# Kernel optimization log

Measured on AMD Instinct MI355X. Metric: run time of the kernel, lower is better.

## Reference

```python
import jax, jax.numpy as jnp
import numpy as np

VOCAB = 1276   # medical-code vocab (one_hot depth for word)
AGE_DEPTH = 91 # one_hot depth for age


def setup_inputs() -> dict:
    key = jax.random.key(0)
    k1, k2, k3 = jax.random.split(key, 3)
    B, S, BAG, D = 64, 128, 40, 768
    word = jax.random.randint(k1, (B, S, BAG), 0, VOCAB)
    age = jax.random.randint(k2, (B, S), 0, AGE_DEPTH)
    W = jax.random.normal(k3, (VOCAB + AGE_DEPTH, D), dtype=jnp.float32) * 0.02
    b = jnp.zeros((D,), dtype=jnp.float32)
    return {"word": word, "age": age, "W": W, "b": b}


def reference(word, age, W, b):
    # word: [B, S, BAG] int codes; age: [B, S] int.
    B, S, BAG = word.shape
    # Multi-hot count-sum: equivalent to reduce_sum(one_hot(word, VOCAB), axis=-2)
    # but computed via scatter-add, avoiding the dense [B,S,BAG,VOCAB] tensor.
    flat = word.reshape(B * S, BAG)
    offs = jnp.arange(B * S, dtype=word.dtype)[:, None] * VOCAB
    counts = (
        jnp.zeros((B * S * VOCAB,), jnp.float32)
        .at[(flat + offs).ravel()]
        .add(1.0)
        .reshape(B, S, VOCAB)
    )
    year = jax.nn.one_hot(age, AGE_DEPTH, dtype=jnp.float32)  # [B, S, 91]
    x = jnp.concatenate([counts, year], axis=-1)              # [B, S, 1367]
    return x @ W + b                                          # [B, S, 768]
```

## Files before the change

kernel.cpp:

```cpp
#include <hip/hip_runtime.h>
#include <hip/hip_fp16.h>

constexpr int BAG       = 40;
constexpr int D         = 768;
constexpr int VOCAB     = 1276;
constexpr int AGE_DEPTH = 91;
constexpr int WROWS     = VOCAB + AGE_DEPTH;

constexpr int COLS = 16;
constexpr int NSLC = D / COLS;
constexpr int RPB  = 256;
constexpr int TPB  = 512;
constexpr int LDSU = 2 * WROWS;

typedef float fx4 __attribute__((ext_vector_type(4)));

__device__ __forceinline__ __half2 u2h(uint u) {
    union { uint u; __half2 h; } v; v.u = u; return v.h;
}
__device__ __forceinline__ ushort f2h(float f) {
    __half h = __float2half(f);
    return *reinterpret_cast<ushort*>(&h);
}

__global__ __launch_bounds__(256) void convert_w_f16(
    const float* __restrict__ W, ushort* __restrict__ Wh, int n)
{
    const int i = (blockIdx.x * 256 + threadIdx.x) * 8;
    if (i + 8 > n) return;
    const float4 a = *reinterpret_cast<const float4*>(W + i);
    const float4 b = *reinterpret_cast<const float4*>(W + i + 4);
    uint4 p;
    p.x = (uint)f2h(a.x) | ((uint)f2h(a.y) << 16);
    p.y = (uint)f2h(a.z) | ((uint)f2h(a.w) << 16);
    p.z = (uint)f2h(b.x) | ((uint)f2h(b.y) << 16);
    p.w = (uint)f2h(b.z) | ((uint)f2h(b.w) << 16);
    *reinterpret_cast<uint4*>(Wh + i) = p;
}

__global__ __launch_bounds__(TPB) void embed_lds_kernel(
    const int* __restrict__ word,
    const int* __restrict__ age,
    const ushort* __restrict__ Wh,
    const float* __restrict__ bias,
    float* __restrict__ out)
{
    __shared__ uint4 lds4[LDSU];

    const int rb = blockIdx.x;
    const int c0 = blockIdx.y * COLS;

    const int t     = threadIdx.x;
    const int chunk = t & 1;
    const int rloc  = t >> 1;
    const int row   = rb * RPB + rloc;

    const int* __restrict__ wrow = word + row * BAG;

    for (int s = t; s < LDSU; s += TPB) {
        const int r = s >> 1;
        const int u = s & 1;
        lds4[u * WROWS + r] =
            *reinterpret_cast<const uint4*>(Wh + (size_t)r * D + c0 + u * 8);
    }

    const int aidx = VOCAB + age[row];
    int cur[8];
    {
        const int4 q0 = *reinterpret_cast<const int4*>(wrow);
        const int4 q1 = *reinterpret_cast<const int4*>(wrow + 4);
        cur[0]=q0.x; cur[1]=q0.y; cur[2]=q0.z; cur[3]=q0.w;
        cur[4]=q1.x; cur[5]=q1.y; cur[6]=q1.z; cur[7]=q1.w;
    }

    __syncthreads();

    const uint4* __restrict__ lp = lds4 + chunk * WROWS;

    __half2 a0 = u2h(0u), a1 = u2h(0u), a2 = u2h(0u), a3 = u2h(0u);

    #pragma unroll
    for (int kb = 0; kb < 5; ++kb) {
        uint4 g[8];
        #pragma unroll
        for (int u = 0; u < 8; ++u)
            g[u] = lp[cur[u]];

        int nxt[8];
        if (kb < 4) {
            const int4 q0 = *reinterpret_cast<const int4*>(wrow + 8 * kb + 8);
            const int4 q1 = *reinterpret_cast<const int4*>(wrow + 8 * kb + 12);
            nxt[0]=q0.x; nxt[1]=q0.y; nxt[2]=q0.z; nxt[3]=q0.w;
            nxt[4]=q1.x; nxt[5]=q1.y; nxt[6]=q1.z; nxt[7]=q1.w;
        }

        #pragma unroll
        for (int u = 0; u < 8; ++u) {
            a0 = __hadd2(a0, u2h(g[u].x));
            a1 = __hadd2(a1, u2h(g[u].y));
            a2 = __hadd2(a2, u2h(g[u].z));
            a3 = __hadd2(a3, u2h(g[u].w));
        }

        if (kb < 4) {
            #pragma unroll
            for (int u = 0; u < 8; ++u) cur[u] = nxt[u];
        }
    }

    {
        const uint4 g = lp[aidx];
        a0 = __hadd2(a0, u2h(g.x));
        a1 = __hadd2(a1, u2h(g.y));
        a2 = __hadd2(a2, u2h(g.z));
        a3 = __hadd2(a3, u2h(g.w));
    }

    const int c = c0 + chunk * 8;
    const float4 b0 = *reinterpret_cast<const float4*>(bias + c);
    const float4 b1 = *reinterpret_cast<const float4*>(bias + c + 4);
    fx4 o0 = { b0.x + __low2float(a0), b0.y + __high2float(a0),
               b0.z + __low2float(a1), b0.w + __high2float(a1) };
    fx4 o1 = { b1.x + __low2float(a2), b1.y + __high2float(a2),
               b1.z + __low2float(a3), b1.w + __high2float(a3) };
    float* op = out + (size_t)row * D + c;
    __builtin_nontemporal_store(o0, reinterpret_cast<fx4*>(op));
    __builtin_nontemporal_store(o1, reinterpret_cast<fx4*>(op + 4));
}

__global__ __launch_bounds__(192) void embedbag_f32_kernel(
    const int* __restrict__ word, const int* __restrict__ age,
    const float* __restrict__ W, const float* __restrict__ bias,
    float* __restrict__ out)
{
    const int row = blockIdx.x;
    const int c   = threadIdx.x * 4;

    float4 acc = *reinterpret_cast<const float4*>(&bias[c]);
    const int* __restrict__ wrow = word + row * BAG;

    #pragma unroll 8
    for (int j = 0; j < BAG; ++j) {
        const int idx = wrow[j];
        const float4 v = *reinterpret_cast<const float4*>(&W[(size_t)idx * D + c]);
        acc.x += v.x; acc.y += v.y; acc.z += v.z; acc.w += v.w;
    }
    {
        const int idx = VOCAB + age[row];
        const float4 v = *reinterpret_cast<const float4*>(&W[(size_t)idx * D + c]);
        acc.x += v.x; acc.y += v.y; acc.z += v.z; acc.w += v.w;
    }
    *reinterpret_cast<float4*>(&out[(size_t)row * D + c]) = acc;
}

extern "C" void kernel_launch(void* const* d_in, const int* in_sizes, int n_in,
                              void* d_out, int out_size, void* d_ws, size_t ws_size,
                              hipStream_t stream) {
    const int* word   = (const int*)d_in[0];
    const int* age    = (const int*)d_in[1];
    const float* W    = (const float*)d_in[2];
    const float* bias = (const float*)d_in[3];
    float* out        = (float*)d_out;

    const int rows = in_sizes[1];

    const size_t need = (size_t)WROWS * D * sizeof(ushort);
    if (rows % RPB == 0 && ws_size >= need) {
        ushort* Wh = (ushort*)d_ws;
        const int n = WROWS * D;
        convert_w_f16<<<(n / 8 + 255) / 256, 256, 0, stream>>>(W, Wh, n);
        dim3 grid(rows / RPB, NSLC);
        embed_lds_kernel<<<grid, TPB, 0, stream>>>(
            word, age, (const ushort*)Wh, bias, out);
    } else {
        embedbag_f32_kernel<<<rows, D / 4, 0, stream>>>(word, age, W, bias, out);
    }
}
```

Baseline: 31.62 us.

## Fuse fp16 weight conversion into double-buffered LDS embedding-bag kernel

Removes the separate W-to-fp16 conversion kernel and its workspace round trip. Each block now converts fp32 W slices to fp16 while staging them into LDS. Each block processes six 16-column slices in sequence, double-buffering LDS so that global loads for the next slice overlap the gather-accumulate of the current one. Word indices are loaded once into registers and reused across slices. In exchange the grid is six times smaller (256 blocks), LDS use doubles, and register pressure rises.

```diff
diff --git a/kernel.cpp b/kernel.cpp
--- a/kernel.cpp
+++ b/kernel.cpp
@@ -7,11 +7,14 @@
 constexpr int AGE_DEPTH = 91;
 constexpr int WROWS     = VOCAB + AGE_DEPTH;
 
-constexpr int COLS = 16;
-constexpr int NSLC = D / COLS;
-constexpr int RPB  = 256;
-constexpr int TPB  = 512;
-constexpr int LDSU = 2 * WROWS;
+constexpr int ROWS_PB = 256;
+constexpr int TPB     = 512;
+constexpr int COLS    = 16;
+constexpr int SPB     = 6;
+constexpr int CPB     = COLS * SPB;
+constexpr int NSG     = D / CPB;
+constexpr int LDSU    = 2 * WROWS;
+constexpr int SITER   = (LDSU + TPB - 1) / TPB;
 
 typedef float fx4 __attribute__((ext_vector_type(4)));
 
@@ -22,110 +25,120 @@
     __half h = __float2half(f);
     return *reinterpret_cast<ushort*>(&h);
 }
-
-__global__ __launch_bounds__(256) void convert_w_f16(
-    const float* __restrict__ W, ushort* __restrict__ Wh, int n)
-{
-    const int i = (blockIdx.x * 256 + threadIdx.x) * 8;
-    if (i + 8 > n) return;
-    const float4 a = *reinterpret_cast<const float4*>(W + i);
-    const float4 b = *reinterpret_cast<const float4*>(W + i + 4);
+__device__ __forceinline__ uint4 pack8(const float4 a, const float4 b) {
     uint4 p;
     p.x = (uint)f2h(a.x) | ((uint)f2h(a.y) << 16);
     p.y = (uint)f2h(a.z) | ((uint)f2h(a.w) << 16);
     p.z = (uint)f2h(b.x) | ((uint)f2h(b.y) << 16);
     p.w = (uint)f2h(b.z) | ((uint)f2h(b.w) << 16);
-    *reinterpret_cast<uint4*>(Wh + i) = p;
+    return p;
 }
 
-__global__ __launch_bounds__(TPB) void embed_lds_kernel(
+__global__ __launch_bounds__(TPB) void embed_dbuf_kernel(
     const int* __restrict__ word,
     const int* __restrict__ age,
-    const ushort* __restrict__ Wh,
+    const float* __restrict__ W,
     const float* __restrict__ bias,
     float* __restrict__ out)
 {
-    __shared__ uint4 lds4[LDSU];
+    __shared__ uint4 buf[2][LDSU];
 
-    const int rb = blockIdx.x;
-    const int c0 = blockIdx.y * COLS;
+    const int rb  = blockIdx.x;
+    const int cb0 = blockIdx.y * CPB;
 
     const int t     = threadIdx.x;
     const int chunk = t & 1;
     const int rloc  = t >> 1;
-    const int row   = rb * RPB + rloc;
+    const int row   = rb * ROWS_PB + rloc;
 
     const int* __restrict__ wrow = word + row * BAG;
+    int idx[BAG];
+    #pragma unroll
+    for (int j = 0; j < BAG; j += 4) {
+        const int4 q = *reinterpret_cast<const int4*>(wrow + j);
+        idx[j] = q.x; idx[j + 1] = q.y; idx[j + 2] = q.z; idx[j + 3] = q.w;
+    }
+    const int aidx = VOCAB + age[row];
 
-    for (int s = t; s < LDSU; s += TPB) {
-        const int r = s >> 1;
-        const int u = s & 1;
-        lds4[u * WROWS + r] =
-            *reinterpret_cast<const uint4*>(Wh + (size_t)r * D + c0 + u * 8);
+    #pragma unroll
+    for (int k = 0; k < SITER; ++k) {
+        const int i = t + k * TPB;
+        if (i < LDSU) {
+            const int r = i >> 1, u = i & 1;
+            const float* src = W + (size_t)r * D + cb0 + u * 8;
+            const float4 a = *reinterpret_cast<const float4*>(src);
+            const float4 b = *reinterpret_cast<const float4*>(src + 4);
+            buf[0][u * WROWS + r] = pack8(a, b);
+        }
     }
-
-    const int aidx = VOCAB + age[row];
-    int cur[8];
-    {
-        const int4 q0 = *reinterpret_cast<const int4*>(wrow);
-        const int4 q1 = *reinterpret_cast<const int4*>(wrow + 4);
-        cur[0]=q0.x; cur[1]=q0.y; cur[2]=q0.z; cur[3]=q0.w;
-        cur[4]=q1.x; cur[5]=q1.y; cur[6]=q1.z; cur[7]=q1.w;
-    }
-
     __syncthreads();
 
-    const uint4* __restrict__ lp = lds4 + chunk * WROWS;
-
-    __half2 a0 = u2h(0u), a1 = u2h(0u), a2 = u2h(0u), a3 = u2h(0u);
-
     #pragma unroll
-    for (int kb = 0; kb < 5; ++kb) {
-        uint4 g[8];
-        #pragma unroll
-        for (int u = 0; u < 8; ++u)
-            g[u] = lp[cur[u]];
-
-        int nxt[8];
-        if (kb < 4) {
-            const int4 q0 = *reinterpret_cast<const int4*>(wrow + 8 * kb + 8);
-            const int4 q1 = *reinterpret_cast<const int4*>(wrow + 8 * kb + 12);
-            nxt[0]=q0.x; nxt[1]=q0.y; nxt[2]=q0.z; nxt[3]=q0.w;
-            nxt[4]=q1.x; nxt[5]=q1.y; nxt[6]=q1.z; nxt[7]=q1.w;
+    for (int s = 0; s < SPB; ++s) {
+        float4 sa[SITER], sb[SITER];
+        if (s + 1 < SPB) {
+            const int cbn = cb0 + (s + 1) * COLS;
+            #pragma unroll
+            for (int k = 0; k < SITER; ++k) {
+                const int i = t + k * TPB;
+                if (i < LDSU) {
+                    const int r = i >> 1, u = i & 1;
+                    const float* src = W + (size_t)r * D + cbn + u * 8;
+                    sa[k] = *reinterpret_cast<const float4*>(src);
+                    sb[k] = *reinterpret_cast<const float4*>(src + 4);
+                }
+            }
         }
 
+        const uint4* __restrict__ lp = buf[s & 1] + chunk * WROWS;
+        __half2 a0 = u2h(0u), a1 = u2h(0u), a2 = u2h(0u), a3 = u2h(0u);
         #pragma unroll
-        for (int u = 0; u < 8; ++u) {
-            a0 = __hadd2(a0, u2h(g[u].x));
-            a1 = __hadd2(a1, u2h(g[u].y));
-            a2 = __hadd2(a2, u2h(g[u].z));
-            a3 = __hadd2(a3, u2h(g[u].w));
+        for (int kb = 0; kb < 5; ++kb) {
+            uint4 g[8];
+            #pragma unroll
+            for (int u = 0; u < 8; ++u)
+                g[u] = lp[idx[kb * 8 + u]];
+            #pragma unroll
+            for (int u = 0; u < 8; ++u) {
+                a0 = __hadd2(a0, u2h(g[u].x));
+                a1 = __hadd2(a1, u2h(g[u].y));
+                a2 = __hadd2(a2, u2h(g[u].z));
+                a3 = __hadd2(a3, u2h(g[u].w));
+            }
+        }
+        {
+            const uint4 g = lp[aidx];
+            a0 = __hadd2(a0, u2h(g.x));
+            a1 = __hadd2(a1, u2h(g.y));
+            a2 = __hadd2(a2, u2h(g.z));
+            a3 = __hadd2(a3, u2h(g.w));
         }
 
-        if (kb < 4) {
+        {
+            const int c = cb0 + s * COLS + chunk * 8;
+            const float4 b0 = *reinterpret_cast<const float4*>(bias + c);
+            const float4 b1 = *reinterpret_cast<const float4*>(bias + c + 4);
+            fx4 o0 = { b0.x + __low2float(a0), b0.y + __high2float(a0),
+                       b0.z + __low2float(a1), b0.w + __high2float(a1) };
+            fx4 o1 = { b1.x + __low2float(a2), b1.y + __high2float(a2),
+                       b1.z + __low2float(a3), b1.w + __high2float(a3) };
+            float* op = out + (size_t)row * D + c;
+            __builtin_nontemporal_store(o0, reinterpret_cast<fx4*>(op));
+            __builtin_nontemporal_store(o1, reinterpret_cast<fx4*>(op + 4));
+        }
+
+        if (s + 1 < SPB) {
             #pragma unroll
-            for (int u = 0; u < 8; ++u) cur[u] = nxt[u];
+            for (int k = 0; k < SITER; ++k) {
+                const int i = t + k * TPB;
+                if (i < LDSU) {
+                    const int r = i >> 1, u = i & 1;
+                    buf[(s + 1) & 1][u * WROWS + r] = pack8(sa[k], sb[k]);
+                }
+            }
         }
+        __syncthreads();
     }
-
-    {
-        const uint4 g = lp[aidx];
-        a0 = __hadd2(a0, u2h(g.x));
-        a1 = __hadd2(a1, u2h(g.y));
-        a2 = __hadd2(a2, u2h(g.z));
-        a3 = __hadd2(a3, u2h(g.w));
-    }
-
-    const int c = c0 + chunk * 8;
-    const float4 b0 = *reinterpret_cast<const float4*>(bias + c);
-    const float4 b1 = *reinterpret_cast<const float4*>(bias + c + 4);
-    fx4 o0 = { b0.x + __low2float(a0), b0.y + __high2float(a0),
-               b0.z + __low2float(a1), b0.w + __high2float(a1) };
-    fx4 o1 = { b1.x + __low2float(a2), b1.y + __high2float(a2),
-               b1.z + __low2float(a3), b1.w + __high2float(a3) };
-    float* op = out + (size_t)row * D + c;
-    __builtin_nontemporal_store(o0, reinterpret_cast<fx4*>(op));
-    __builtin_nontemporal_store(o1, reinterpret_cast<fx4*>(op + 4));
 }
 
 __global__ __launch_bounds__(192) void embedbag_f32_kernel(
@@ -164,14 +177,9 @@
 
     const int rows = in_sizes[1];
 
-    const size_t need = (size_t)WROWS * D * sizeof(ushort);
-    if (rows % RPB == 0 && ws_size >= need) {
-        ushort* Wh = (ushort*)d_ws;
-        const int n = WROWS * D;
-        convert_w_f16<<<(n / 8 + 255) / 256, 256, 0, stream>>>(W, Wh, n);
-        dim3 grid(rows / RPB, NSLC);
-        embed_lds_kernel<<<grid, TPB, 0, stream>>>(
-            word, age, (const ushort*)Wh, bias, out);
+    if (rows % ROWS_PB == 0) {
+        dim3 grid(rows / ROWS_PB, NSG);
+        embed_dbuf_kernel<<<grid, TPB, 0, stream>>>(word, age, W, bias, out);
     } else {
         embedbag_f32_kernel<<<rows, D / 4, 0, stream>>>(word, age, W, bias, out);
     }
```

Result: faster. 29.37 us (-7.1%).
